# Kernel tuning notes

Hardware: AMD Instinct MI355X
Metric: run time of the kernel (lower is better)

The kernel has to match this reference:

```python
import jax, jax.numpy as jnp
import numpy as np

B, N, C = 128, 1024, 1
N_TIMES = 2
NUM_SUBSTEPS = 279  # trunc(dt_Output/dt_sub)+1 for default params


def setup_inputs() -> dict:
    key = jax.random.key(0)
    # small amplitude: d_to_u multiplies spectrum by k (up to N/2), keep CFL stable
    x = jax.random.normal(key, (B, N, C), dtype=jnp.float32) * 1e-3
    return {
        "x": x,
        "nu_para": jnp.float32(-3.0),
        "dt_Output_para": jnp.float32(-3.0),
        "cRatio_para": jnp.float32(0.1),
        "nTimes": N_TIMES,
        "num_substeps": NUM_SUBSTEPS,
    }


def _forward(x, nu_para, dt_Output_para, cRatio_para, nTimes, num_substeps):
    n = x.shape[1]
    L = 2.0 * np.pi
    k = (2.0 * np.pi / L) * jnp.arange(n // 2 + 1, dtype=jnp.float32)  # [n//2+1]
    ik = 1j * k

    # reparameterized physical params (sigmoid squashing, as in the torch module)
    nu = jax.nn.sigmoid(nu_para) * (0.5 - 0.01) + 0.01
    dt_out = jax.nn.sigmoid(dt_Output_para) * (0.1 - 0.001) + 0.001
    cR = jax.nn.sigmoid(cRatio_para) * (2.0 - 0.5) + 0.5

    d = jnp.transpose(x, (0, 2, 1))  # [B, C, N]
    # d_to_u: u = irfft(1j * rfft(d) * k)
    u = jnp.fft.irfft(1j * jnp.fft.rfft(d) * k, n=n)

    dt = dt_out / num_substeps
    # q = 1 - dt*cR*(k + nu*(1j*k)^2) ; (1j*k)^2 = -k^2 so q is real-valued
    q = 1.0 - dt * cR * (k - nu * k * k)

    def substep(u, _):
        uhat = jnp.fft.rfft(u)
        u2hat = jnp.fft.rfft(0.5 * u * u)
        u_new = jnp.fft.irfft((uhat - dt * ik * u2hat) / q, n=n)
        return u_new, None

    def outer(u, _):
        u, _ = jax.lax.scan(substep, u, None, length=num_substeps)
        return u, u

    _, usol = jax.lax.scan(outer, u, None, length=nTimes)  # [T, B, C, N]
    T = usol.shape[0]
    # torch.cat(usol, dim=1): [B, T*C, N] with time-major ordering
    usol = jnp.moveaxis(usol, 0, 1).reshape(usol.shape[1], T * usol.shape[2], n)

    # u_to_d: d_hat = -1j*rfft(u); d_hat[...,1:] /= k[1:]; d_hat[...,0] = 0
    d_hat = -1j * jnp.fft.rfft(usol)
    safe_k = jnp.where(k > 0, k, 1.0)
    d_hat = jnp.where(k > 0, d_hat / safe_k, jnp.zeros((), dtype=d_hat.dtype))
    dsol = jnp.fft.irfft(d_hat, n=n)  # [B, T*C, N]

    return jnp.transpose(dsol, (0, 2, 1))  # [B, N, T*C]


def reference(x, nu_para, dt_Output_para, cRatio_para, nTimes, num_substeps):
    return _forward(x, nu_para, dt_Output_para, cRatio_para, nTimes, num_substeps)
```

## Files before the change

### kernel.cpp

```cpp
#include <hip/hip_runtime.h>
#include <math.h>

#define NFFT 1024
#define BLK  512

template <int CTRL>
__device__ __forceinline__ float dppf(float v) {
    return __int_as_float(__builtin_amdgcn_update_dpp(
        0, __float_as_int(v), CTRL, 0xF, 0xF, true));
}
__device__ __forceinline__ float qx1(float v) { return dppf<0xB1>(v); }
__device__ __forceinline__ float qx2(float v) { return dppf<0x4E>(v); }
__device__ __forceinline__ float qx3(float v) { return dppf<0x1B>(v); }
__device__ __forceinline__ float xr4(float v) { return dppf<0x1B>(dppf<0x141>(v)); }
__device__ __forceinline__ float xr8(float v) { return dppf<0x128>(v); }

__device__ __forceinline__ void pswap16(float v, float& lo, float& hi) {
    auto r = __builtin_amdgcn_permlane16_swap(__float_as_int(v), __float_as_int(v),
                                              false, false);
    lo = __int_as_float(r[0]);
    hi = __int_as_float(r[1]);
}
__device__ __forceinline__ void pswap32(float v, float& lo, float& hi) {
    auto r = __builtin_amdgcn_permlane32_swap(__float_as_int(v), __float_as_int(v),
                                              false, false);
    lo = __int_as_float(r[0]);
    hi = __int_as_float(r[1]);
}

__global__ __launch_bounds__(BLK, 2)
void siva_kernel(const float* __restrict__ x,
                 const float* __restrict__ nu_p,
                 const float* __restrict__ dto_p,
                 const float* __restrict__ cr_p,
                 const int* __restrict__ nt_p,
                 const int* __restrict__ ns_p,
                 float* __restrict__ out) {
    __shared__ float4 bufF[BLK];
    __shared__ float4 bufI[BLK];

    const int tt = threadIdx.x;
    const int b  = blockIdx.x;
    const int l  = tt & 63;
    const int w  = tt >> 6;
    const int R  = (int)(__brev((unsigned)l) >> 26);

    const int nT   = nt_p[0];
    const int nsub = ns_p[0];

    const float nu  = (1.0f / (1.0f + expf(-nu_p[0])))  * (0.5f - 0.01f)  + 0.01f;
    const float dto = (1.0f / (1.0f + expf(-dto_p[0]))) * (0.1f - 0.001f) + 0.001f;
    const float cR  = (1.0f / (1.0f + expf(-cr_p[0])))  * (2.0f - 0.5f)   + 0.5f;
    const float dt   = dto / (float)nsub;
    const float dtcR = dt * cR;

    float2 T10;
    { const float a = (float)tt * (1.0f / 512.0f);
      T10 = make_float2(cospif(a), -sinpif(a)); }

    const float pm = (w & 1) ? -1.0f : 1.0f;
    float2 c4w, w8w, rotf;
    { const float aw = 0.5f * (float)w;
      c4w = make_float2(cospif(aw), -sinpif(aw));
      const float aw8 = 0.25f * (float)w;
      w8w = make_float2(cospif(aw8), -sinpif(aw8));
      const float ar = (float)(l * w) * (1.0f / 256.0f);
      rotf = make_float2(cospif(ar), -sinpif(ar)); }

    float2 D8[8];
    #pragma unroll
    for (int j = 0; j < 8; ++j) {
        const float ai = (float)(w * j) * 0.25f + (float)(l * j) * (1.0f / 256.0f);
        D8[j] = make_float2(cospif(ai), sinpif(ai));
    }

    float2 wf[6]; float sg[6]; float2 wi[6];
    #pragma unroll
    for (int s = 0; s < 6; ++s) {
        const int h = 32 >> s;
        const int lm = l & (h - 1);
        const bool hif = (l & h) != 0;
        const float a = (float)(lm * (32 / h)) * (1.0f / 32.0f);
        wf[s] = hif ? make_float2(cospif(a), -sinpif(a)) : make_float2(1.0f, 0.0f);
        sg[s] = hif ? -1.0f : 1.0f;
        const int h2 = 1 << s;
        const int lm2 = l & (h2 - 1);
        const float a2 = (float)lm2 / (float)h2;
        float2 wb = make_float2(cospif(a2), sinpif(a2));
        if ((l & h2) != 0) { wb.x = -wb.x; wb.y = -wb.y; }
        wi[s] = wb;
    }
    const bool m1 = (l & 1) != 0, m2 = (l & 2) != 0,
               m4 = (l & 4) != 0, m8 = (l & 8) != 0;

    float2 cai[2], cbi[2];
    #pragma unroll
    for (int s = 2; s <= 3; ++s) {
        const bool hif = (l & (1 << s)) != 0;
        cai[s - 2] = hif ? wi[s] : make_float2(1.0f, 0.0f);
        cbi[s - 2] = hif ? make_float2(1.0f, 0.0f) : wi[s];
    }

    float Sc[2], csn[2], si[2];
    #pragma unroll
    for (int p = 0; p < 2; ++p) {
        const int k = 16 * R + 2 * w + p;
        const float kk = (k <= 512) ? (float)k : (float)(k - 1024);
        const float ka = fabsf(kk);
        const float q  = 1.0f - dtcR * (ka - nu * ka * ka);
        const float a  = (1.0f / q) * (1.0f / 1024.0f);
        const float kkS = (k == 0 || k == 512) ? 0.0f : kk;
        Sc[p]  = a * (1.0f - dt * kkS);
        csn[p] = (k == 0) ? 0.0f : (1.0f / (1024.0f * kk));
        si[p]  = kk * (1.0f / 1024.0f);
    }

    float2 Cq[2][4];
    {
        auto compose = [&](float2* o, const float2* bb, const float2* aa) {
            #pragma unroll
            for (int e = 0; e < 4; ++e) {
                float cx = 0.0f, cy = 0.0f;
                #pragma unroll
                for (int d = 0; d < 4; ++d) {
                    const float ax = __shfl_xor(aa[d ^ e].x, d);
                    const float ay = __shfl_xor(aa[d ^ e].y, d);
                    cx = fmaf(bb[d].x, ax, fmaf(-bb[d].y, ay, cx));
                    cy = fmaf(bb[d].x, ay, fmaf(bb[d].y, ax, cy));
                }
                o[e] = make_float2(cx, cy);
            }
        };
        const float2 one = make_float2(1.0f, 0.0f);
        const float2 zer = make_float2(0.0f, 0.0f);
        float2 Arow[4] = { make_float2(wf[4].x * sg[4], wf[4].y * sg[4]), zer,
                           wf[4], zer };
        float2 Brow[4] = { make_float2(sg[5], 0.0f), one, zer, zer };
        float2 Erow[4] = { m1 ? wi[0] : one, m1 ? one : wi[0], zer, zer };
        float2 Frow[4] = { m2 ? wi[1] : one, zer, m2 ? one : wi[1], zer };
        float2 M1[4], M2[4], M3[4];
        compose(M1, Brow, Arow);
        #pragma unroll
        for (int p = 0; p < 2; ++p) {
            #pragma unroll
            for (int e = 0; e < 4; ++e)
                M2[e] = make_float2(Sc[p] * M1[e].x, Sc[p] * M1[e].y);
            compose(M3, Erow, M2);
            compose(Cq[p], Frow, M3);
        }
    }

    auto fwd_s = [&](float2& zz, float bx, float by, int s) {
        const float tx = fmaf(sg[s], zz.x, bx);
        const float ty = fmaf(sg[s], zz.y, by);
        zz.x = tx * wf[s].x - ty * wf[s].y;
        zz.y = tx * wf[s].y + ty * wf[s].x;
    };
    auto inv_s = [&](float2& zz, float bx, float by, int s, bool hi) {
        const float px = hi ? zz.x : bx, py = hi ? zz.y : by;
        const float qx = hi ? bx : zz.x, qy = hi ? by : zz.y;
        zz.x = qx + px * wi[s].x - py * wi[s].y;
        zz.y = qy + px * wi[s].y + py * wi[s].x;
    };

    auto lane_fwd4 = [&](float2 z[2]) {
        #pragma unroll
        for (int r = 0; r < 2; ++r) {
            float lox, hix, loy, hiy;
            pswap32(z[r].x, lox, hix); pswap32(z[r].y, loy, hiy);
            const float tx = fmaf(sg[0], hix, lox);
            const float ty = fmaf(sg[0], hiy, loy);
            z[r].x = tx * wf[0].x - ty * wf[0].y;
            z[r].y = tx * wf[0].y + ty * wf[0].x;
        }
        #pragma unroll
        for (int r = 0; r < 2; ++r) {
            float lox, hix, loy, hiy;
            pswap16(z[r].x, lox, hix); pswap16(z[r].y, loy, hiy);
            const float tx = fmaf(sg[1], hix, lox);
            const float ty = fmaf(sg[1], hiy, loy);
            z[r].x = tx * wf[1].x - ty * wf[1].y;
            z[r].y = tx * wf[1].y + ty * wf[1].x;
        }
        #pragma unroll
        for (int r = 0; r < 2; ++r) fwd_s(z[r], xr8(z[r].x), xr8(z[r].y), 2);
        #pragma unroll
        for (int r = 0; r < 2; ++r) fwd_s(z[r], xr4(z[r].x), xr4(z[r].y), 3);
    };
    auto lane_inv4 = [&](float2 z[2]) {
        #pragma unroll
        for (int r = 0; r < 2; ++r) {
            const float px = xr4(z[r].x), py = xr4(z[r].y);
            const float nx = fmaf(cai[0].x, z[r].x, fmaf(-cai[0].y, z[r].y,
                             fmaf(cbi[0].x, px, -cbi[0].y * py)));
            const float ny = fmaf(cai[0].x, z[r].y, fmaf(cai[0].y, z[r].x,
                             fmaf(cbi[0].x, py, cbi[0].y * px)));
            z[r] = make_float2(nx, ny);
        }
        #pragma unroll
        for (int r = 0; r < 2; ++r) {
            const float px = xr8(z[r].x), py = xr8(z[r].y);
            const float nx = fmaf(cai[1].x, z[r].x, fmaf(-cai[1].y, z[r].y,
                             fmaf(cbi[1].x, px, -cbi[1].y * py)));
            const float ny = fmaf(cai[1].x, z[r].y, fmaf(cai[1].y, z[r].x,
                             fmaf(cbi[1].x, py, cbi[1].y * px)));
            z[r] = make_float2(nx, ny);
        }
        #pragma unroll
        for (int r = 0; r < 2; ++r) {
            float lox, hix, loy, hiy;
            pswap16(z[r].x, lox, hix); pswap16(z[r].y, loy, hiy);
            z[r].x = fmaf(wi[4].x, hix, fmaf(-wi[4].y, hiy, lox));
            z[r].y = fmaf(wi[4].x, hiy, fmaf( wi[4].y, hix, loy));
        }
        #pragma unroll
        for (int r = 0; r < 2; ++r) {
            float lox, hix, loy, hiy;
            pswap32(z[r].x, lox, hix); pswap32(z[r].y, loy, hiy);
            z[r].x = fmaf(wi[5].x, hix, fmaf(-wi[5].y, hiy, lox));
            z[r].y = fmaf(wi[5].x, hiy, fmaf( wi[5].y, hix, loy));
        }
    };

    auto stageQuadC = [&](float2 z[2]) {
        #pragma unroll
        for (int p = 0; p < 2; ++p) {
            const float x1 = qx1(z[p].x), y1 = qx1(z[p].y);
            const float x2 = qx2(z[p].x), y2 = qx2(z[p].y);
            const float x3 = qx3(z[p].x), y3 = qx3(z[p].y);
            float nx = Cq[p][0].x * z[p].x - Cq[p][0].y * z[p].y;
            float ny = Cq[p][0].x * z[p].y + Cq[p][0].y * z[p].x;
            nx = fmaf(Cq[p][1].x, x1, fmaf(-Cq[p][1].y, y1, nx));
            ny = fmaf(Cq[p][1].x, y1, fmaf( Cq[p][1].y, x1, ny));
            nx = fmaf(Cq[p][2].x, x2, fmaf(-Cq[p][2].y, y2, nx));
            ny = fmaf(Cq[p][2].x, y2, fmaf( Cq[p][2].y, x2, ny));
            nx = fmaf(Cq[p][3].x, x3, fmaf(-Cq[p][3].y, y3, nx));
            ny = fmaf(Cq[p][3].x, y3, fmaf( Cq[p][3].y, x3, ny));
            z[p] = make_float2(nx, ny);
        }
    };

    auto fwd_head = [&](float2 z[2]) {
        const float2 A  = make_float2(z[0].x + z[1].x, z[0].y + z[1].y);
        const float2 Dm = make_float2(z[0].x - z[1].x, z[0].y - z[1].y);
        const float2 Bc = make_float2(Dm.x * T10.x - Dm.y * T10.y,
                                      Dm.x * T10.y + Dm.y * T10.x);
        bufF[tt] = make_float4(A.x, A.y, Bc.x, Bc.y);
        __syncthreads();
        float a0x, a0y, a0z, a0w, a1x, a1y, a1z, a1w;
        float a2x, a2y, a2z, a2w, a3x, a3y, a3z, a3w;
        {
            const float4 u0 = bufF[l],        u4 = bufF[256 + l];
            a0x = fmaf(pm, u4.x, u0.x);  a0y = fmaf(pm, u4.y, u0.y);
            a0z = fmaf(pm, u4.z, u0.z);  a0w = fmaf(pm, u4.w, u0.w);
        }
        {
            const float4 u2 = bufF[128 + l],  u6 = bufF[384 + l];
            a1x = fmaf(pm, u6.x, u2.x);  a1y = fmaf(pm, u6.y, u2.y);
            a1z = fmaf(pm, u6.z, u2.z);  a1w = fmaf(pm, u6.w, u2.w);
        }
        {
            const float4 u1 = bufF[64 + l],   u5 = bufF[320 + l];
            a2x = fmaf(pm, u5.x, u1.x);  a2y = fmaf(pm, u5.y, u1.y);
            a2z = fmaf(pm, u5.z, u1.z);  a2w = fmaf(pm, u5.w, u1.w);
        }
        {
            const float4 u3 = bufF[192 + l],  u7 = bufF[448 + l];
            a3x = fmaf(pm, u7.x, u3.x);  a3y = fmaf(pm, u7.y, u3.y);
            a3z = fmaf(pm, u7.z, u3.z);  a3w = fmaf(pm, u7.w, u3.w);
        }
        {
            const float Ex = fmaf(c4w.x, a1x, fmaf(-c4w.y, a1y, a0x));
            const float Ey = fmaf(c4w.x, a1y, fmaf( c4w.y, a1x, a0y));
            const float Fx = fmaf(c4w.x, a3x, fmaf(-c4w.y, a3y, a2x));
            const float Fy = fmaf(c4w.x, a3y, fmaf( c4w.y, a3x, a2y));
            const float Sx = fmaf(w8w.x, Fx, fmaf(-w8w.y, Fy, Ex));
            const float Sy = fmaf(w8w.x, Fy, fmaf( w8w.y, Fx, Ey));
            z[0] = make_float2(Sx * rotf.x - Sy * rotf.y,
                               Sx * rotf.y + Sy * rotf.x);
        }
        {
            const float Ex = fmaf(c4w.x, a1z, fmaf(-c4w.y, a1w, a0z));
            const float Ey = fmaf(c4w.x, a1w, fmaf( c4w.y, a1z, a0w));
            const float Fx = fmaf(c4w.x, a3z, fmaf(-c4w.y, a3w, a2z));
            const float Fy = fmaf(c4w.x, a3w, fmaf( c4w.y, a3z, a2w));
            const float Sx = fmaf(w8w.x, Fx, fmaf(-w8w.y, Fy, Ex));
            const float Sy = fmaf(w8w.x, Fy, fmaf( w8w.y, Fx, Ey));
            z[1] = make_float2(Sx * rotf.x - Sy * rotf.y,
                               Sx * rotf.y + Sy * rotf.x);
        }
        lane_fwd4(z);
    };

    auto inv_tail = [&](float2 z[2], float& u0o, float& u1o) {
        lane_inv4(z);
        bufI[tt] = make_float4(z[0].x, z[0].y, z[1].x, z[1].y);
        __syncthreads();
        float vAx, vBx, vBy;
        { const float4 v0 = bufI[l];
          vAx = v0.x; vBx = v0.z; vBy = v0.w; }
        #pragma unroll
        for (int j = 1; j < 8; ++j) {
            const float4 v = bufI[64 * j + l];
            vAx = fmaf(D8[j].x, v.x, vAx);  vAx = fmaf(-D8[j].y, v.y, vAx);
            vBx = fmaf(D8[j].x, v.z, vBx);  vBx = fmaf(-D8[j].y, v.w, vBx);
            vBy = fmaf(D8[j].x, v.w, vBy);  vBy = fmaf(D8[j].y, v.z, vBy);
        }
        const float re = vBx * T10.x + vBy * T10.y;
        u0o = vAx + re;
        u1o = vAx - re;
    };

    float2 z[2];
    float u0, u1;
    z[0] = make_float2(x[b * NFFT + tt], 0.0f);
    z[1] = make_float2(x[b * NFFT + tt + 512], 0.0f);
    fwd_head(z);
    #pragma unroll
    for (int r = 0; r < 2; ++r) fwd_s(z[r], qx2(z[r].x), qx2(z[r].y), 4);
    #pragma unroll
    for (int r = 0; r < 2; ++r) fwd_s(z[r], qx1(z[r].x), qx1(z[r].y), 5);
    #pragma unroll
    for (int p = 0; p < 2; ++p) {
        const float zx = z[p].x, zy = z[p].y;
        z[p] = make_float2(-zy * si[p], zx * si[p]);
    }
    #pragma unroll
    for (int r = 0; r < 2; ++r) inv_s(z[r], qx1(z[r].x), qx1(z[r].y), 0, m1);
    #pragma unroll
    for (int r = 0; r < 2; ++r) inv_s(z[r], qx2(z[r].x), qx2(z[r].y), 1, m2);
    inv_tail(z, u0, u1);

    for (int ot = 0; ot < nT; ++ot) {
        for (int ss = 0; ss < nsub; ++ss) {
            z[0] = make_float2(u0, 0.5f * u0 * u0);
            z[1] = make_float2(u1, 0.5f * u1 * u1);
            fwd_head(z);
            stageQuadC(z);
            inv_tail(z, u0, u1);
        }
        z[0] = make_float2(u0, 0.0f);
        z[1] = make_float2(u1, 0.0f);
        fwd_head(z);
        #pragma unroll
        for (int r = 0; r < 2; ++r) fwd_s(z[r], qx2(z[r].x), qx2(z[r].y), 4);
        #pragma unroll
        for (int r = 0; r < 2; ++r) fwd_s(z[r], qx1(z[r].x), qx1(z[r].y), 5);
        #pragma unroll
        for (int p = 0; p < 2; ++p) {
            const float zx = z[p].x, zy = z[p].y;
            z[p] = make_float2(zy * csn[p], -zx * csn[p]);
        }
        #pragma unroll
        for (int r = 0; r < 2; ++r) inv_s(z[r], qx1(z[r].x), qx1(z[r].y), 0, m1);
        #pragma unroll
        for (int r = 0; r < 2; ++r) inv_s(z[r], qx2(z[r].x), qx2(z[r].y), 1, m2);
        float d0, d1;
        inv_tail(z, d0, d1);
        out[(b * NFFT + tt) * nT + ot]       = d0;
        out[(b * NFFT + tt + 512) * nT + ot] = d1;
    }
}

extern "C" void kernel_launch(void* const* d_in, const int* in_sizes, int n_in,
                              void* d_out, int out_size, void* d_ws, size_t ws_size,
                              hipStream_t stream) {
    const float* x     = (const float*)d_in[0];
    const float* nu_p  = (const float*)d_in[1];
    const float* dto_p = (const float*)d_in[2];
    const float* cr_p  = (const float*)d_in[3];
    const int*   nt_p  = (const int*)d_in[4];
    const int*   ns_p  = (const int*)d_in[5];
    float* out = (float*)d_out;

    const int B = in_sizes[0] / NFFT;
    siva_kernel<<<B, BLK, 0, stream>>>(x, nu_p, dto_p, cr_p, nt_p, ns_p, out);
}
```

Measured before the change: 709.4 us.

## Fold spectral multiply into 2-lane stencil, move stage 4 into butterflies

The fused spectral operator was a 4-lane complex stencil that combined the last two forward stages, the pointwise multiply and the first two inverse stages. It now covers only the last forward and first inverse stage, a 2-lane real-coefficient stencil using one qx1 DPP swap and two FMAs per component. Forward stage 4 and inverse stage 1 move back into the explicit butterfly helpers. The aim is to cut DPP cross-lane moves and complex multiplies in the inner substep loop, at the cost of two extra explicit butterfly stages.

```diff
diff --git a/kernel.cpp b/kernel.cpp
--- a/kernel.cpp
+++ b/kernel.cpp
@@ -11,7 +11,6 @@
 }
 __device__ __forceinline__ float qx1(float v) { return dppf<0xB1>(v); }
 __device__ __forceinline__ float qx2(float v) { return dppf<0x4E>(v); }
-__device__ __forceinline__ float qx3(float v) { return dppf<0x1B>(v); }
 __device__ __forceinline__ float xr4(float v) { return dppf<0x1B>(dppf<0x141>(v)); }
 __device__ __forceinline__ float xr8(float v) { return dppf<0x128>(v); }
 
@@ -90,15 +89,14 @@
         if ((l & h2) != 0) { wb.x = -wb.x; wb.y = -wb.y; }
         wi[s] = wb;
     }
-    const bool m1 = (l & 1) != 0, m2 = (l & 2) != 0,
-               m4 = (l & 4) != 0, m8 = (l & 8) != 0;
-
-    float2 cai[2], cbi[2];
-    #pragma unroll
-    for (int s = 2; s <= 3; ++s) {
+    const bool m1 = (l & 1) != 0, m2 = (l & 2) != 0;
+
+    float2 cai[3], cbi[3];
+    #pragma unroll
+    for (int s = 1; s <= 3; ++s) {
         const bool hif = (l & (1 << s)) != 0;
-        cai[s - 2] = hif ? wi[s] : make_float2(1.0f, 0.0f);
-        cbi[s - 2] = hif ? make_float2(1.0f, 0.0f) : wi[s];
+        cai[s - 1] = hif ? wi[s] : make_float2(1.0f, 0.0f);
+        cbi[s - 1] = hif ? make_float2(1.0f, 0.0f) : wi[s];
     }
 
     float Sc[2], csn[2], si[2];
@@ -114,41 +112,14 @@
         csn[p] = (k == 0) ? 0.0f : (1.0f / (1024.0f * kk));
         si[p]  = kk * (1.0f / 1024.0f);
     }
-
-    float2 Cq[2][4];
-    {
-        auto compose = [&](float2* o, const float2* bb, const float2* aa) {
-            #pragma unroll
-            for (int e = 0; e < 4; ++e) {
-                float cx = 0.0f, cy = 0.0f;
-                #pragma unroll
-                for (int d = 0; d < 4; ++d) {
-                    const float ax = __shfl_xor(aa[d ^ e].x, d);
-                    const float ay = __shfl_xor(aa[d ^ e].y, d);
-                    cx = fmaf(bb[d].x, ax, fmaf(-bb[d].y, ay, cx));
-                    cy = fmaf(bb[d].x, ay, fmaf(bb[d].y, ax, cy));
-                }
-                o[e] = make_float2(cx, cy);
-            }
-        };
-        const float2 one = make_float2(1.0f, 0.0f);
-        const float2 zer = make_float2(0.0f, 0.0f);
-        float2 Arow[4] = { make_float2(wf[4].x * sg[4], wf[4].y * sg[4]), zer,
-                           wf[4], zer };
-        float2 Brow[4] = { make_float2(sg[5], 0.0f), one, zer, zer };
-        float2 Erow[4] = { m1 ? wi[0] : one, m1 ? one : wi[0], zer, zer };
-        float2 Frow[4] = { m2 ? wi[1] : one, zer, m2 ? one : wi[1], zer };
-        float2 M1[4], M2[4], M3[4];
-        compose(M1, Brow, Arow);
-        #pragma unroll
-        for (int p = 0; p < 2; ++p) {
-            #pragma unroll
-            for (int e = 0; e < 4; ++e)
-                M2[e] = make_float2(Sc[p] * M1[e].x, Sc[p] * M1[e].y);
-            compose(M3, Erow, M2);
-            compose(Cq[p], Frow, M3);
-        }
-    }
+    float A2[2], B2[2];
+    { const float sg1 = (l & 1) ? -1.0f : 1.0f;
+      #pragma unroll
+      for (int p = 0; p < 2; ++p) {
+          const float so = __shfl_xor(Sc[p], 1);
+          A2[p] = Sc[p] + so;
+          B2[p] = sg1 * (Sc[p] - so);
+      } }
 
     auto fwd_s = [&](float2& zz, float bx, float by, int s) {
         const float tx = fmaf(sg[s], zz.x, bx);
@@ -163,7 +134,7 @@
         zz.y = qy + px * wi[s].y + py * wi[s].x;
     };
 
-    auto lane_fwd4 = [&](float2 z[2]) {
+    auto lane_fwd5 = [&](float2 z[2]) {
         #pragma unroll
         for (int r = 0; r < 2; ++r) {
             float lox, hix, loy, hiy;
@@ -186,11 +157,13 @@
         for (int r = 0; r < 2; ++r) fwd_s(z[r], xr8(z[r].x), xr8(z[r].y), 2);
         #pragma unroll
         for (int r = 0; r < 2; ++r) fwd_s(z[r], xr4(z[r].x), xr4(z[r].y), 3);
-    };
-    auto lane_inv4 = [&](float2 z[2]) {
-        #pragma unroll
-        for (int r = 0; r < 2; ++r) {
-            const float px = xr4(z[r].x), py = xr4(z[r].y);
+        #pragma unroll
+        for (int r = 0; r < 2; ++r) fwd_s(z[r], qx2(z[r].x), qx2(z[r].y), 4);
+    };
+    auto lane_inv5 = [&](float2 z[2]) {
+        #pragma unroll
+        for (int r = 0; r < 2; ++r) {
+            const float px = qx2(z[r].x), py = qx2(z[r].y);
             const float nx = fmaf(cai[0].x, z[r].x, fmaf(-cai[0].y, z[r].y,
                              fmaf(cbi[0].x, px, -cbi[0].y * py)));
             const float ny = fmaf(cai[0].x, z[r].y, fmaf(cai[0].y, z[r].x,
@@ -199,7 +172,7 @@
         }
         #pragma unroll
         for (int r = 0; r < 2; ++r) {
-            const float px = xr8(z[r].x), py = xr8(z[r].y);
+            const float px = xr4(z[r].x), py = xr4(z[r].y);
             const float nx = fmaf(cai[1].x, z[r].x, fmaf(-cai[1].y, z[r].y,
                              fmaf(cbi[1].x, px, -cbi[1].y * py)));
             const float ny = fmaf(cai[1].x, z[r].y, fmaf(cai[1].y, z[r].x,
@@ -208,6 +181,15 @@
         }
         #pragma unroll
         for (int r = 0; r < 2; ++r) {
+            const float px = xr8(z[r].x), py = xr8(z[r].y);
+            const float nx = fmaf(cai[2].x, z[r].x, fmaf(-cai[2].y, z[r].y,
+                             fmaf(cbi[2].x, px, -cbi[2].y * py)));
+            const float ny = fmaf(cai[2].x, z[r].y, fmaf(cai[2].y, z[r].x,
+                             fmaf(cbi[2].x, py, cbi[2].y * px)));
+            z[r] = make_float2(nx, ny);
+        }
+        #pragma unroll
+        for (int r = 0; r < 2; ++r) {
             float lox, hix, loy, hiy;
             pswap16(z[r].x, lox, hix); pswap16(z[r].y, loy, hiy);
             z[r].x = fmaf(wi[4].x, hix, fmaf(-wi[4].y, hiy, lox));
@@ -219,24 +201,6 @@
             pswap32(z[r].x, lox, hix); pswap32(z[r].y, loy, hiy);
             z[r].x = fmaf(wi[5].x, hix, fmaf(-wi[5].y, hiy, lox));
             z[r].y = fmaf(wi[5].x, hiy, fmaf( wi[5].y, hix, loy));
-        }
-    };
-
-    auto stageQuadC = [&](float2 z[2]) {
-        #pragma unroll
-        for (int p = 0; p < 2; ++p) {
-            const float x1 = qx1(z[p].x), y1 = qx1(z[p].y);
-            const float x2 = qx2(z[p].x), y2 = qx2(z[p].y);
-            const float x3 = qx3(z[p].x), y3 = qx3(z[p].y);
-            float nx = Cq[p][0].x * z[p].x - Cq[p][0].y * z[p].y;
-            float ny = Cq[p][0].x * z[p].y + Cq[p][0].y * z[p].x;
-            nx = fmaf(Cq[p][1].x, x1, fmaf(-Cq[p][1].y, y1, nx));
-            ny = fmaf(Cq[p][1].x, y1, fmaf( Cq[p][1].y, x1, ny));
-            nx = fmaf(Cq[p][2].x, x2, fmaf(-Cq[p][2].y, y2, nx));
-            ny = fmaf(Cq[p][2].x, y2, fmaf( Cq[p][2].y, x2, ny));
-            nx = fmaf(Cq[p][3].x, x3, fmaf(-Cq[p][3].y, y3, nx));
-            ny = fmaf(Cq[p][3].x, y3, fmaf( Cq[p][3].y, x3, ny));
-            z[p] = make_float2(nx, ny);
         }
     };
 
@@ -289,11 +253,11 @@
             z[1] = make_float2(Sx * rotf.x - Sy * rotf.y,
                                Sx * rotf.y + Sy * rotf.x);
         }
-        lane_fwd4(z);
+        lane_fwd5(z);
     };
 
     auto inv_tail = [&](float2 z[2], float& u0o, float& u1o) {
-        lane_inv4(z);
+        lane_inv5(z);
         bufI[tt] = make_float4(z[0].x, z[0].y, z[1].x, z[1].y);
         __syncthreads();
         float vAx, vBx, vBy;
@@ -317,8 +281,6 @@
     z[1] = make_float2(x[b * NFFT + tt + 512], 0.0f);
     fwd_head(z);
     #pragma unroll
-    for (int r = 0; r < 2; ++r) fwd_s(z[r], qx2(z[r].x), qx2(z[r].y), 4);
-    #pragma unroll
     for (int r = 0; r < 2; ++r) fwd_s(z[r], qx1(z[r].x), qx1(z[r].y), 5);
     #pragma unroll
     for (int p = 0; p < 2; ++p) {
@@ -327,8 +289,6 @@
     }
     #pragma unroll
     for (int r = 0; r < 2; ++r) inv_s(z[r], qx1(z[r].x), qx1(z[r].y), 0, m1);
-    #pragma unroll
-    for (int r = 0; r < 2; ++r) inv_s(z[r], qx2(z[r].x), qx2(z[r].y), 1, m2);
     inv_tail(z, u0, u1);
 
     for (int ot = 0; ot < nT; ++ot) {
@@ -336,15 +296,18 @@
             z[0] = make_float2(u0, 0.5f * u0 * u0);
             z[1] = make_float2(u1, 0.5f * u1 * u1);
             fwd_head(z);
-            stageQuadC(z);
+            #pragma unroll
+            for (int p = 0; p < 2; ++p) {
+                const float px = qx1(z[p].x), py = qx1(z[p].y);
+                z[p].x = fmaf(A2[p], z[p].x, B2[p] * px);
+                z[p].y = fmaf(A2[p], z[p].y, B2[p] * py);
+            }
             inv_tail(z, u0, u1);
         }
         z[0] = make_float2(u0, 0.0f);
         z[1] = make_float2(u1, 0.0f);
         fwd_head(z);
         #pragma unroll
-        for (int r = 0; r < 2; ++r) fwd_s(z[r], qx2(z[r].x), qx2(z[r].y), 4);
-        #pragma unroll
         for (int r = 0; r < 2; ++r) fwd_s(z[r], qx1(z[r].x), qx1(z[r].y), 5);
         #pragma unroll
         for (int p = 0; p < 2; ++p) {
@@ -353,8 +316,6 @@
         }
         #pragma unroll
         for (int r = 0; r < 2; ++r) inv_s(z[r], qx1(z[r].x), qx1(z[r].y), 0, m1);
-        #pragma unroll
-        for (int r = 0; r < 2; ++r) inv_s(z[r], qx2(z[r].x), qx2(z[r].y), 1, m2);
         float d0, d1;
         inv_tail(z, d0, d1);
         out[(b * NFFT + tt) * nT + ot]       = d0;
```

Result: no change. 704.2 us (-0.7%).
